# Optimization experiments

Measured on AMD Instinct MI355X. Metric: run time of the kernel, lower is better.

The kernel has to match this reference:

```python
import jax, jax.numpy as jnp
import numpy as np

N_HEAD = 16
EPS = 1e-5
ROPE_BASE = 10000.0


def setup_inputs() -> dict:
    key = jax.random.key(0)
    ks = jax.random.split(key, 6)
    B, T, C = 2, 2048, 1024
    s = 0.02  # typical GPT init scale
    return {
        "x": jax.random.normal(ks[0], (B, T, C), dtype=jnp.float32),
        "wq": jax.random.normal(ks[1], (C, C), dtype=jnp.float32) * s,
        "wk": jax.random.normal(ks[2], (C, C), dtype=jnp.float32) * s,
        "wv": jax.random.normal(ks[3], (C, C), dtype=jnp.float32) * s,
        "wproj": jax.random.normal(ks[4], (C, C), dtype=jnp.float32) * s,
        "g_rms": jnp.ones((C // N_HEAD,), dtype=jnp.float32),
    }


def reference(x, wq, wk, wv, wproj, g_rms):
    B, T, C = x.shape
    H = N_HEAD
    hd = C // H

    # QKV projections (torch Linear: y = x @ W.T), split into heads -> [B,T,H,hd]
    q = (x @ wq.T).reshape(B, T, H, hd)
    k = (x @ wk.T).reshape(B, T, H, hd)
    v = (x @ wv.T).reshape(B, T, H, hd)

    # RMSNorm over head_dim on q and k
    def rms(t):
        var = jnp.mean(t * t, axis=-1, keepdims=True) + EPS
        return g_rms * (t * jax.lax.rsqrt(var))

    q, k = rms(q), rms(k)

    # Rotary embeddings: cos/sin cached in bf16 in the original -> bf16 round-trip
    inv_freq = 1.0 / (ROPE_BASE ** (jnp.arange(0, hd, 2, dtype=jnp.float32) / hd))
    freqs = jnp.outer(jnp.arange(T, dtype=jnp.float32), inv_freq)  # [T, hd/2]
    cos = jnp.cos(freqs).astype(jnp.bfloat16).astype(jnp.float32)[None, :, None, :]
    sin = jnp.sin(freqs).astype(jnp.bfloat16).astype(jnp.float32)[None, :, None, :]

    def rope(u):
        d = hd // 2
        u1, u2 = u[..., :d], u[..., d:]
        return jnp.concatenate([u1 * cos + u2 * sin, -u1 * sin + u2 * cos], axis=-1)

    q, k = rope(q), rope(k)

    # Attention: float ones attn_mask => constant +1.0 bias (softmax-invariant);
    # NOT causal (is_causal defaults False); dropout_p = 0.
    qh = q.transpose(0, 2, 1, 3)  # [B,H,T,hd]
    kh = k.transpose(0, 2, 1, 3)
    vh = v.transpose(0, 2, 1, 3)
    scale = 1.0 / jnp.sqrt(jnp.float32(hd))
    scores = jnp.einsum('bhtd,bhsd->bhts', qh, kh) * scale + 1.0  # [B,H,T,T]
    attn = jax.nn.softmax(scores, axis=-1)
    y = jnp.einsum('bhts,bhsd->bhtd', attn, vh)

    y = y.transpose(0, 2, 1, 3).reshape(B, T, C)
    return y @ wproj.T
```

## Files before the change

### kernel.cpp

```cpp
#include <hip/hip_runtime.h>
#include <hip/hip_bf16.h>
#include <stdint.h>

typedef __attribute__((ext_vector_type(8))) short short8;
typedef __attribute__((ext_vector_type(4))) float f32x4;
typedef __attribute__((ext_vector_type(16))) float f32x16;
typedef __attribute__((ext_vector_type(4))) unsigned short ushort4v;
typedef __attribute__((ext_vector_type(4))) unsigned int uint4v;

#define TT 2048
#define HH 16
#define CCdim 1024
#define BT 4096
#define LOG2E 1.44269504088896f

__device__ inline unsigned short f2bf(float f) {
  unsigned u = __float_as_uint(f);
  u += 0x7FFF + ((u >> 16) & 1);
  return (unsigned short)(u >> 16);
}
__device__ inline float bf2f(unsigned short s) {
  return __uint_as_float(((unsigned)s) << 16);
}
__device__ inline unsigned pack2(float a, float b) {
  return (unsigned)f2bf(a) | ((unsigned)f2bf(b) << 16);
}
__device__ inline unsigned cvtpk(float lo, float hi) {
  unsigned r;
  asm("v_cvt_pk_bf16_f32 %0, %1, %2" : "=v"(r) : "v"(lo), "v"(hi));
  return r;
}
__device__ inline void plswap(unsigned &a, unsigned &b) {
  asm("v_permlane32_swap_b32 %0, %1" : "+v"(a), "+v"(b));
}

__device__ inline void gload16(const unsigned short* g, unsigned short* l) {
  __builtin_amdgcn_global_load_lds((const __attribute__((address_space(1))) void*)g,
                                   (__attribute__((address_space(3))) void*)l, 16, 0, 0);
}

#define VMB(N) do { asm volatile("s_waitcnt vmcnt(" #N ")" ::: "memory"); \
                    __builtin_amdgcn_s_barrier(); \
                    __builtin_amdgcn_sched_barrier(0); } while (0)

__global__ __launch_bounds__(256) void prep(const float* __restrict__ x, const float* __restrict__ wq,
                     const float* __restrict__ wk, const float* __restrict__ wv,
                     const float* __restrict__ wp, unsigned short* __restrict__ xb,
                     unsigned short* __restrict__ wqkv, unsigned short* __restrict__ wpb,
                     float2* __restrict__ tab) {
  long idx = ((long)blockIdx.x * 256 + threadIdx.x) * 4;
  const long NX = (long)BT * CCdim;
  const long NW = (long)CCdim * CCdim;
  auto cvt4 = [](const float* src, unsigned short* dst, long off) {
    float4 v = *(const float4*)(src + off);
    ushort4v o = { f2bf(v.x), f2bf(v.y), f2bf(v.z), f2bf(v.w) };
    *(ushort4v*)(dst + off) = o;
  };
  if (idx < NX) { cvt4(x, xb, idx); return; }
  idx -= NX;
  if (idx < NW) { cvt4(wq, wqkv, idx); return; }
  idx -= NW;
  if (idx < NW) { cvt4(wk, wqkv + NW, idx); return; }
  idx -= NW;
  if (idx < NW) { cvt4(wv, wqkv + 2 * NW, idx); return; }
  idx -= NW;
  if (idx < NW) { cvt4(wp, wpb, idx); return; }
  idx -= NW;
  if (idx < (long)TT * 32) {
#pragma unroll
    for (int j = 0; j < 4; ++j) {
      long e = idx + j;
      int t = (int)(e >> 5), i = (int)(e & 31);
      float invf = powf(10000.0f, -(float)i / 32.0f);
      float a = (float)t * invf;
      tab[e] = make_float2(bf2f(f2bf(cosf(a))), bf2f(f2bf(sinf(a))));
    }
  }
}

__global__ __launch_bounds__(256) void gemm_qkv(const unsigned short* __restrict__ A,
                                                const unsigned short* __restrict__ W,
                                                const float* __restrict__ g,
                                                const float2* __restrict__ tab,
                                                unsigned short* __restrict__ Qh,
                                                unsigned short* __restrict__ Kp,
                                                unsigned short* __restrict__ Vp) {
  __shared__ __align__(16) char smem[49152];
  unsigned short* const S0 = (unsigned short*)smem;
  unsigned short* const S1 = S0 + 8192;
  unsigned short* const S2 = S0 + 16384;
  typedef unsigned short (*Earr)[64][68];
  Earr E = (Earr)smem;
  const int K = 1024;
  const int tid = threadIdx.x;
  const int lane = tid & 63;
  const int wid = tid >> 6;
  const int wr = wid >> 1, wc = wid & 1;
  const int m0 = blockIdx.y * 128;
  const int n0 = blockIdx.x * 128;

  f32x4 acc[4][4] = {};

  const int srow0 = tid >> 2;
  const int cgrp = tid & 3;
  const int cd = (cgrp ^ ((srow0 >> 1) & 3)) * 8;
  const unsigned short* Arow0 = A + (long)(m0 + srow0) * K + cd;
  const unsigned short* Arow1 = A + (long)(m0 + srow0 + 64) * K + cd;
  const unsigned short* Wrow0 = W + (long)(n0 + srow0) * K + cd;
  const unsigned short* Wrow1 = W + (long)(n0 + srow0 + 64) * K + cd;

  auto stage = [&](unsigned short* Ab, int kt) {
    const int kof = kt * 32;
    gload16(Arow0 + kof, Ab + wid * 512);
    gload16(Arow1 + kof, Ab + 2048 + wid * 512);
    gload16(Wrow0 + kof, Ab + 4096 + wid * 512);
    gload16(Wrow1 + kof, Ab + 6144 + wid * 512);
  };
  auto compute = [&](const unsigned short* Ab) {
    const unsigned short* Wb = Ab + 4096;
    short8 af[4], bf[4];
#pragma unroll
    for (int mi = 0; mi < 4; ++mi) {
      int r = wr * 64 + mi * 16 + (lane & 15);
      af[mi] = *(const short8*)&Ab[r * 32 + (((lane >> 4) ^ ((r >> 1) & 3)) * 8)];
    }
#pragma unroll
    for (int nj = 0; nj < 4; ++nj) {
      int r = wc * 64 + nj * 16 + (lane & 15);
      bf[nj] = *(const short8*)&Wb[r * 32 + (((lane >> 4) ^ ((r >> 1) & 3)) * 8)];
    }
#pragma unroll
    for (int mi = 0; mi < 4; ++mi)
#pragma unroll
      for (int nj = 0; nj < 4; ++nj)
        acc[mi][nj] = __builtin_amdgcn_mfma_f32_16x16x32_bf16(af[mi], bf[nj], acc[mi][nj], 0, 0, 0);
  };

  stage(S0, 0);
  stage(S1, 1);
  for (int tb = 0; tb < 30; tb += 3) {
    VMB(4); stage(S2, tb + 2); compute(S0);
    VMB(4); stage(S0, tb + 3); compute(S1);
    VMB(4); stage(S1, tb + 4); compute(S2);
  }
  VMB(4); compute(S0);
  VMB(0); compute(S1);
  __syncthreads();

  const int type = blockIdx.x >> 3;
  const int c0 = n0 + wc * 64;
  const int b = m0 >> 11;
  const int t0w = (m0 & 2047) + wr * 64;
  const int bh = b * 16 + ((c0 >> 6) & 15);
  const int cl = lane & 15;
  const int hi4 = lane >> 4;

  if (type < 2) {
    float gv0 = g[cl], gv1 = g[cl + 16], gv2 = g[cl + 32], gv3 = g[cl + 48];
    const float qs = (type == 0) ? 0.125f * LOG2E : 1.0f;
#pragma unroll
    for (int mi = 0; mi < 4; ++mi)
#pragma unroll
      for (int j = 0; j < 4; ++j) {
        float x0 = acc[mi][0][j], x1 = acc[mi][1][j], x2 = acc[mi][2][j], x3 = acc[mi][3][j];
        float ss = x0 * x0 + x1 * x1 + x2 * x2 + x3 * x3;
        ss += __shfl_xor(ss, 1); ss += __shfl_xor(ss, 2);
        ss += __shfl_xor(ss, 4); ss += __shfl_xor(ss, 8);
        float ri = rsqrtf(ss * (1.0f / 64.0f) + 1e-5f);
        float xn0 = x0 * ri * gv0, xn1 = x1 * ri * gv1;
        float xn2 = x2 * ri * gv2, xn3 = x3 * ri * gv3;
        int t = t0w + mi * 16 + 4 * hi4 + j;
        float2 cs0 = tab[t * 32 + cl];
        float2 cs1 = tab[t * 32 + cl + 16];
        int lr = mi * 16 + 4 * hi4 + j;
        E[wid][lr][cl]      = f2bf((xn0 * cs0.x + xn2 * cs0.y) * qs);
        E[wid][lr][cl + 16] = f2bf((xn1 * cs1.x + xn3 * cs1.y) * qs);
        E[wid][lr][cl + 32] = f2bf((xn2 * cs0.x - xn0 * cs0.y) * qs);
        E[wid][lr][cl + 48] = f2bf((xn3 * cs1.x - xn1 * cs1.y) * qs);
      }
  } else {
#pragma unroll
    for (int mi = 0; mi < 4; ++mi)
#pragma unroll
      for (int j = 0; j < 4; ++j) {
        int lr = mi * 16 + 4 * hi4 + j;
        E[wid][lr][cl]      = f2bf(acc[mi][0][j]);
        E[wid][lr][cl + 16] = f2bf(acc[mi][1][j]);
        E[wid][lr][cl + 32] = f2bf(acc[mi][2][j]);
        E[wid][lr][cl + 48] = f2bf(acc[mi][3][j]);
      }
  }
  __syncthreads();

  if (type == 0) {
    for (int row = 0; row < 64; ++row) {
      int t = t0w + row;
      Qh[((long)bh * TT + t) * 64 + lane] = E[wid][row][lane];
    }
  } else if (type == 1) {
    for (int row = 0; row < 64; ++row) {
      int t = t0w + row;
      Kp[(((long)bh * 64 + (t >> 5)) * 4 + (lane >> 4)) * 512
         + ((t & 31) + 32 * ((lane >> 3) & 1)) * 8 + (lane & 7)] = E[wid][row][lane];
    }
  } else {
    unsigned short* base = Vp + ((long)bh * 64 + (t0w >> 5)) * 2048;
#pragma unroll
    for (int it = 0; it < 8; ++it) {
      int id = it * 64 + lane;
      int cc = it & 1, sd = (it >> 1) & 1, ttloc = (it >> 2) & 1;
      int d = sd * 32 + (lane & 31);
      int tl = ttloc * 32 + cc * 16 + (lane >> 5) * 8;
      short8 o;
#pragma unroll
      for (int jj = 0; jj < 8; ++jj) o[jj] = (short)E[wid][tl + jj][d];
      *(short8*)(base + (long)id * 8) = o;
    }
  }
}

__global__ __launch_bounds__(256) void gemm_bt(const unsigned short* __restrict__ A,
                                               const unsigned short* __restrict__ W,
                                               float* __restrict__ C, int ldc) {
  __shared__ __align__(16) unsigned short Sbuf[3][8192];
  unsigned short* const S0 = &Sbuf[0][0];
  unsigned short* const S1 = &Sbuf[1][0];
  unsigned short* const S2 = &Sbuf[2][0];
  const int K = 1024;
  const int tid = threadIdx.x;
  const int lane = tid & 63;
  const int wid = tid >> 6;
  const int wr = wid >> 1, wc = wid & 1;
  const int m0 = blockIdx.y * 128;
  const int n0 = blockIdx.x * 128;

  f32x4 acc[4][4] = {};

  const int srow0 = tid >> 2;
  const int cgrp = tid & 3;
  const int cd = (cgrp ^ ((srow0 >> 1) & 3)) * 8;
  const unsigned short* Arow0 = A + (long)(m0 + srow0) * K + cd;
  const unsigned short* Arow1 = A + (long)(m0 + srow0 + 64) * K + cd;
  const unsigned short* Wrow0 = W + (long)(n0 + srow0) * K + cd;
  const unsigned short* Wrow1 = W + (long)(n0 + srow0 + 64) * K + cd;

  auto stage = [&](unsigned short* Ab, int kt) {
    const int kof = kt * 32;
    gload16(Arow0 + kof, Ab + wid * 512);
    gload16(Arow1 + kof, Ab + 2048 + wid * 512);
    gload16(Wrow0 + kof, Ab + 4096 + wid * 512);
    gload16(Wrow1 + kof, Ab + 6144 + wid * 512);
  };
  auto compute = [&](const unsigned short* Ab) {
    const unsigned short* Wb = Ab + 4096;
    short8 af[4], bf[4];
#pragma unroll
    for (int mi = 0; mi < 4; ++mi) {
      int r = wr * 64 + mi * 16 + (lane & 15);
      af[mi] = *(const short8*)&Ab[r * 32 + (((lane >> 4) ^ ((r >> 1) & 3)) * 8)];
    }
#pragma unroll
    for (int nj = 0; nj < 4; ++nj) {
      int r = wc * 64 + nj * 16 + (lane & 15);
      bf[nj] = *(const short8*)&Wb[r * 32 + (((lane >> 4) ^ ((r >> 1) & 3)) * 8)];
    }
#pragma unroll
    for (int mi = 0; mi < 4; ++mi)
#pragma unroll
      for (int nj = 0; nj < 4; ++nj)
        acc[mi][nj] = __builtin_amdgcn_mfma_f32_16x16x32_bf16(af[mi], bf[nj], acc[mi][nj], 0, 0, 0);
  };

  stage(S0, 0);
  stage(S1, 1);
  for (int tb = 0; tb < 30; tb += 3) {
    VMB(4); stage(S2, tb + 2); compute(S0);
    VMB(4); stage(S0, tb + 3); compute(S1);
    VMB(4); stage(S1, tb + 4); compute(S2);
  }
  VMB(4); compute(S0);
  VMB(0); compute(S1);

#pragma unroll
  for (int mi = 0; mi < 4; ++mi)
#pragma unroll
    for (int nj = 0; nj < 4; ++nj)
#pragma unroll
      for (int j = 0; j < 4; ++j) {
        int rr = m0 + wr * 64 + mi * 16 + 4 * (lane >> 4) + j;
        int ncol = n0 + wc * 64 + nj * 16 + (lane & 15);
        C[(long)rr * ldc + ncol] = acc[mi][nj][j];
      }
}

__global__ __launch_bounds__(256, 3) void attn(const unsigned short* __restrict__ Qh,
                                               const unsigned short* __restrict__ Kp,
                                               const unsigned short* __restrict__ Vp,
                                               float* __restrict__ Opart,
                                               float* __restrict__ L) {
  const int lane = threadIdx.x & 63;
  const int wid = threadIdx.x >> 6;
  int bid = blockIdx.x;
  bid = (bid & 7) * 128 + (bid >> 3);
  const int w = bid * 4 + wid;
  const int qt = w & 63;
  const int half = (w >> 6) & 1;
  const int bh = w >> 7;
  const long bhT = (long)bh * TT;
  const int q0 = qt * 32;
  const int l31 = lane & 31;
  const int hk = (lane >> 5) * 8;

  short8 qf[4];
  {
    const unsigned short* qp = Qh + (bhT + q0 + l31) * 64 + hk;
#pragma unroll
    for (int c = 0; c < 4; ++c) qf[c] = *(const short8*)(qp + c * 16);
  }

  const unsigned short* kp = Kp + ((long)(bh * 64 + half * 32)) * 2048 + lane * 8;
  const unsigned short* vp = Vp + ((long)(bh * 64 + half * 32)) * 2048 + lane * 8;

  f32x16 oacc0 = {}, oacc1 = {};
  float ell = 0.f;

  short8 kA[4], vA0[2], vA1[2], kB[4], vB0[2], vB1[2];
#pragma unroll
  for (int c = 0; c < 4; ++c) kA[c] = *(const short8*)(kp + c * 512);
#pragma unroll
  for (int c = 0; c < 2; ++c) {
    vA0[c] = *(const short8*)(vp + c * 512);
    vA1[c] = *(const short8*)(vp + 1024 + c * 512);
  }

  auto body = [&](short8 (&kc)[4], short8 (&v0c)[2], short8 (&v1c)[2],
                  short8 (&knx)[4], short8 (&v0n)[2], short8 (&v1n)[2], int tn) {
    const unsigned short* kpn = kp + tn * 2048;
    const unsigned short* vpn = vp + tn * 2048;
#pragma unroll
    for (int c = 0; c < 4; ++c) knx[c] = *(const short8*)(kpn + c * 512);
#pragma unroll
    for (int c = 0; c < 2; ++c) {
      v0n[c] = *(const short8*)(vpn + c * 512);
      v1n[c] = *(const short8*)(vpn + 1024 + c * 512);
    }

    __builtin_amdgcn_s_setprio(1);
    f32x16 s = {};
#pragma unroll
    for (int c = 0; c < 4; ++c)
      s = __builtin_amdgcn_mfma_f32_32x32x16_bf16(kc[c], qf[c], s, 0, 0, 0);
    __builtin_amdgcn_s_setprio(0);

#pragma unroll
    for (int r = 0; r < 16; ++r) s[r] = __builtin_amdgcn_exp2f(s[r]);
    float t0 = s[0] + s[1], t1 = s[2] + s[3], t2s = s[4] + s[5], t3 = s[6] + s[7];
    float t4 = s[8] + s[9], t5 = s[10] + s[11], t6 = s[12] + s[13], t7 = s[14] + s[15];
    t0 += t1; t2s += t3; t4 += t5; t6 += t7;
    ell += (t0 + t2s) + (t4 + t6);

    unsigned a0 = cvtpk(s[0], s[1]),   a1 = cvtpk(s[2], s[3]);
    unsigned a2 = cvtpk(s[4], s[5]),   a3 = cvtpk(s[6], s[7]);
    unsigned a4 = cvtpk(s[8], s[9]),   a5 = cvtpk(s[10], s[11]);
    unsigned a6 = cvtpk(s[12], s[13]), a7 = cvtpk(s[14], s[15]);
    plswap(a0, a2); plswap(a1, a3); plswap(a4, a6); plswap(a5, a7);
    uint4v f0 = { a0, a1, a2, a3 };
    uint4v f1 = { a4, a5, a6, a7 };
    short8 pf0 = __builtin_bit_cast(short8, f0);
    short8 pf1 = __builtin_bit_cast(short8, f1);

    __builtin_amdgcn_s_setprio(1);
    oacc0 = __builtin_amdgcn_mfma_f32_32x32x16_bf16(v0c[0], pf0, oacc0, 0, 0, 0);
    oacc0 = __builtin_amdgcn_mfma_f32_32x32x16_bf16(v0c[1], pf1, oacc0, 0, 0, 0);
    oacc1 = __builtin_amdgcn_mfma_f32_32x32x16_bf16(v1c[0], pf0, oacc1, 0, 0, 0);
    oacc1 = __builtin_amdgcn_mfma_f32_32x32x16_bf16(v1c[1], pf1, oacc1, 0, 0, 0);
    __builtin_amdgcn_s_setprio(0);
  };

  for (int t = 0; t < 32; t += 2) {
    int t1 = t + 1;
    int t2 = (t < 30) ? (t + 2) : 31;
    body(kA, vA0, vA1, kB, vB0, vB1, t1);
    body(kB, vB0, vB1, kA, vA0, vA1, t2);
  }

  float ellf = ell + __shfl_xor(ell, 32);
  const long prow = (long)(half * 32 + bh) * TT + q0 + l31;
  float* orow = Opart + prow * 64;
  const int dhalf = 4 * (lane >> 5);
#pragma unroll
  for (int i = 0; i < 8; ++i) {
    int d = (2 * i & 3) + 8 * (i >> 1) + dhalf;
    *(float2*)&orow[d]      = make_float2(oacc0[2 * i], oacc0[2 * i + 1]);
    *(float2*)&orow[32 + d] = make_float2(oacc1[2 * i], oacc1[2 * i + 1]);
  }
  if (lane < 32) L[prow] = ellf;
}

__global__ __launch_bounds__(256) void combine(const float* __restrict__ Opart,
                                               const float* __restrict__ L,
                                               unsigned short* __restrict__ Y) {
  const long HALF = (long)32 * TT * 64;
  int idx = blockIdx.x * 256 + threadIdx.x;
  int row = idx >> 5;
  int d = (idx & 31) * 2;
  float2 o0 = *(const float2*)&Opart[(long)row * 64 + d];
  float2 o1 = *(const float2*)&Opart[HALF + (long)row * 64 + d];
  float rinv = 1.0f / (L[row] + L[65536 + row]);
  float ox = (o0.x + o1.x) * rinv;
  float oy = (o0.y + o1.y) * rinv;
  int bh = row >> 11, qrow = row & (TT - 1);
  int b = bh >> 4, h = bh & 15;
  *(unsigned*)&Y[((long)(b * TT + qrow)) * CCdim + h * 64 + d] = pack2(ox, oy);
}

extern "C" void kernel_launch(void* const* d_in, const int* in_sizes, int n_in,
                              void* d_out, int out_size, void* d_ws, size_t ws_size,
                              hipStream_t stream) {
  const float* x  = (const float*)d_in[0];
  const float* wq = (const float*)d_in[1];
  const float* wk = (const float*)d_in[2];
  const float* wv = (const float*)d_in[3];
  const float* wp = (const float*)d_in[4];
  const float* g  = (const float*)d_in[5];

  char* w = (char*)d_ws;
  unsigned short* xb   = (unsigned short*)w; w += (long)BT * CCdim * 2;
  unsigned short* wqkv = (unsigned short*)w; w += (long)3 * CCdim * CCdim * 2;
  unsigned short* wpb  = (unsigned short*)w; w += (long)CCdim * CCdim * 2;
  unsigned short* qh   = (unsigned short*)w; w += (long)BT * CCdim * 2;
  unsigned short* kp   = (unsigned short*)w; w += (long)BT * CCdim * 2;
  unsigned short* vp   = (unsigned short*)w; w += (long)BT * CCdim * 2;
  unsigned short* yb   = (unsigned short*)w; w += (long)BT * CCdim * 2;
  float2* tab          = (float2*)w;         w += (long)TT * 32 * 8;
  float* Opart         = (float*)w;          w += (long)64 * TT * 64 * 4;
  float* Lbuf          = (float*)w;          w += (long)64 * TT * 4;

  long total = ((long)BT * CCdim + 4L * CCdim * CCdim + (long)TT * 32) / 4;
  int pblocks = (int)((total + 255) / 256);
  prep<<<pblocks, 256, 0, stream>>>(x, wq, wk, wv, wp, xb, wqkv, wpb, tab);
  gemm_qkv<<<dim3(24, 32), 256, 0, stream>>>(xb, wqkv, g, tab, qh, kp, vp);
  attn<<<1024, 256, 0, stream>>>(qh, kp, vp, Opart, Lbuf);
  combine<<<8192, 256, 0, stream>>>(Opart, Lbuf, yb);
  gemm_bt<<<dim3(8, 32), 256, 0, stream>>>(yb, wpb, (float*)d_out, 1024);
}
```

Baseline: 134.2 us.

## Process two 32-row query tiles per wave in attention to reuse K/V loads

Each attention wave now handles 64 query rows instead of 32, holding two sets of Q fragments and four output accumulators, so every K/V fragment loaded from global memory feeds twice as many MFMAs. The grid is halved, the block remapping is adjusted, and launch bounds drop from 3 to 2 waves per SIMD to make room for the extra registers. This targets the global K/V load traffic per unit of compute, at the cost of lower occupancy and fewer blocks to hide latency.

```diff
diff --git a/kernel.cpp b/kernel.cpp
--- a/kernel.cpp
+++ b/kernel.cpp
@@ -293,7 +293,7 @@
       }
 }
 
-__global__ __launch_bounds__(256, 3) void attn(const unsigned short* __restrict__ Qh,
+__global__ __launch_bounds__(256, 2) void attn(const unsigned short* __restrict__ Qh,
                                                const unsigned short* __restrict__ Kp,
                                                const unsigned short* __restrict__ Vp,
                                                float* __restrict__ Opart,
@@ -301,28 +301,31 @@
   const int lane = threadIdx.x & 63;
   const int wid = threadIdx.x >> 6;
   int bid = blockIdx.x;
-  bid = (bid & 7) * 128 + (bid >> 3);
+  bid = (bid & 7) * 64 + (bid >> 3);
   const int w = bid * 4 + wid;
-  const int qt = w & 63;
-  const int half = (w >> 6) & 1;
-  const int bh = w >> 7;
+  const int qt = w & 31;
+  const int half = (w >> 5) & 1;
+  const int bh = w >> 6;
   const long bhT = (long)bh * TT;
-  const int q0 = qt * 32;
+  const int q0 = qt * 64;
   const int l31 = lane & 31;
   const int hk = (lane >> 5) * 8;
 
-  short8 qf[4];
+  short8 qf[4], qg[4];
   {
     const unsigned short* qp = Qh + (bhT + q0 + l31) * 64 + hk;
 #pragma unroll
-    for (int c = 0; c < 4; ++c) qf[c] = *(const short8*)(qp + c * 16);
+    for (int c = 0; c < 4; ++c) {
+      qf[c] = *(const short8*)(qp + c * 16);
+      qg[c] = *(const short8*)(qp + 2048 + c * 16);
+    }
   }
 
   const unsigned short* kp = Kp + ((long)(bh * 64 + half * 32)) * 2048 + lane * 8;
   const unsigned short* vp = Vp + ((long)(bh * 64 + half * 32)) * 2048 + lane * 8;
 
-  f32x16 oacc0 = {}, oacc1 = {};
-  float ell = 0.f;
+  f32x16 oacc0 = {}, oacc1 = {}, oacc2 = {}, oacc3 = {};
+  float ell = 0.f, ell2 = 0.f;
 
   short8 kA[4], vA0[2], vA1[2], kB[4], vB0[2], vB1[2];
 #pragma unroll
@@ -346,18 +349,30 @@
     }
 
     __builtin_amdgcn_s_setprio(1);
-    f32x16 s = {};
-#pragma unroll
-    for (int c = 0; c < 4; ++c)
-      s = __builtin_amdgcn_mfma_f32_32x32x16_bf16(kc[c], qf[c], s, 0, 0, 0);
+    f32x16 s = {}, s2 = {};
+#pragma unroll
+    for (int c = 0; c < 4; ++c) {
+      s  = __builtin_amdgcn_mfma_f32_32x32x16_bf16(kc[c], qf[c], s, 0, 0, 0);
+      s2 = __builtin_amdgcn_mfma_f32_32x32x16_bf16(kc[c], qg[c], s2, 0, 0, 0);
+    }
     __builtin_amdgcn_s_setprio(0);
 
 #pragma unroll
     for (int r = 0; r < 16; ++r) s[r] = __builtin_amdgcn_exp2f(s[r]);
-    float t0 = s[0] + s[1], t1 = s[2] + s[3], t2s = s[4] + s[5], t3 = s[6] + s[7];
-    float t4 = s[8] + s[9], t5 = s[10] + s[11], t6 = s[12] + s[13], t7 = s[14] + s[15];
-    t0 += t1; t2s += t3; t4 += t5; t6 += t7;
-    ell += (t0 + t2s) + (t4 + t6);
+#pragma unroll
+    for (int r = 0; r < 16; ++r) s2[r] = __builtin_amdgcn_exp2f(s2[r]);
+    {
+      float t0 = s[0] + s[1], t1 = s[2] + s[3], t2s = s[4] + s[5], t3 = s[6] + s[7];
+      float t4 = s[8] + s[9], t5 = s[10] + s[11], t6 = s[12] + s[13], t7 = s[14] + s[15];
+      t0 += t1; t2s += t3; t4 += t5; t6 += t7;
+      ell += (t0 + t2s) + (t4 + t6);
+    }
+    {
+      float t0 = s2[0] + s2[1], t1 = s2[2] + s2[3], t2s = s2[4] + s2[5], t3 = s2[6] + s2[7];
+      float t4 = s2[8] + s2[9], t5 = s2[10] + s2[11], t6 = s2[12] + s2[13], t7 = s2[14] + s2[15];
+      t0 += t1; t2s += t3; t4 += t5; t6 += t7;
+      ell2 += (t0 + t2s) + (t4 + t6);
+    }
 
     unsigned a0 = cvtpk(s[0], s[1]),   a1 = cvtpk(s[2], s[3]);
     unsigned a2 = cvtpk(s[4], s[5]),   a3 = cvtpk(s[6], s[7]);
@@ -369,11 +384,25 @@
     short8 pf0 = __builtin_bit_cast(short8, f0);
     short8 pf1 = __builtin_bit_cast(short8, f1);
 
+    unsigned b0 = cvtpk(s2[0], s2[1]),   b1 = cvtpk(s2[2], s2[3]);
+    unsigned b2 = cvtpk(s2[4], s2[5]),   b3 = cvtpk(s2[6], s2[7]);
+    unsigned b4 = cvtpk(s2[8], s2[9]),   b5 = cvtpk(s2[10], s2[11]);
+    unsigned b6 = cvtpk(s2[12], s2[13]), b7 = cvtpk(s2[14], s2[15]);
+    plswap(b0, b2); plswap(b1, b3); plswap(b4, b6); plswap(b5, b7);
+    uint4v g0 = { b0, b1, b2, b3 };
+    uint4v g1 = { b4, b5, b6, b7 };
+    short8 pg0 = __builtin_bit_cast(short8, g0);
+    short8 pg1 = __builtin_bit_cast(short8, g1);
+
     __builtin_amdgcn_s_setprio(1);
     oacc0 = __builtin_amdgcn_mfma_f32_32x32x16_bf16(v0c[0], pf0, oacc0, 0, 0, 0);
     oacc0 = __builtin_amdgcn_mfma_f32_32x32x16_bf16(v0c[1], pf1, oacc0, 0, 0, 0);
     oacc1 = __builtin_amdgcn_mfma_f32_32x32x16_bf16(v1c[0], pf0, oacc1, 0, 0, 0);
     oacc1 = __builtin_amdgcn_mfma_f32_32x32x16_bf16(v1c[1], pf1, oacc1, 0, 0, 0);
+    oacc2 = __builtin_amdgcn_mfma_f32_32x32x16_bf16(v0c[0], pg0, oacc2, 0, 0, 0);
+    oacc2 = __builtin_amdgcn_mfma_f32_32x32x16_bf16(v0c[1], pg1, oacc2, 0, 0, 0);
+    oacc3 = __builtin_amdgcn_mfma_f32_32x32x16_bf16(v1c[0], pg0, oacc3, 0, 0, 0);
+    oacc3 = __builtin_amdgcn_mfma_f32_32x32x16_bf16(v1c[1], pg1, oacc3, 0, 0, 0);
     __builtin_amdgcn_s_setprio(0);
   };
 
@@ -384,17 +413,21 @@
     body(kB, vB0, vB1, kA, vA0, vA1, t2);
   }
 
-  float ellf = ell + __shfl_xor(ell, 32);
+  float ellf  = ell + __shfl_xor(ell, 32);
+  float ellf2 = ell2 + __shfl_xor(ell2, 32);
   const long prow = (long)(half * 32 + bh) * TT + q0 + l31;
-  float* orow = Opart + prow * 64;
+  float* orow  = Opart + prow * 64;
+  float* orow2 = orow + 32 * 64;
   const int dhalf = 4 * (lane >> 5);
 #pragma unroll
   for (int i = 0; i < 8; ++i) {
     int d = (2 * i & 3) + 8 * (i >> 1) + dhalf;
-    *(float2*)&orow[d]      = make_float2(oacc0[2 * i], oacc0[2 * i + 1]);
-    *(float2*)&orow[32 + d] = make_float2(oacc1[2 * i], oacc1[2 * i + 1]);
-  }
-  if (lane < 32) L[prow] = ellf;
+    *(float2*)&orow[d]       = make_float2(oacc0[2 * i], oacc0[2 * i + 1]);
+    *(float2*)&orow[32 + d]  = make_float2(oacc1[2 * i], oacc1[2 * i + 1]);
+    *(float2*)&orow2[d]      = make_float2(oacc2[2 * i], oacc2[2 * i + 1]);
+    *(float2*)&orow2[32 + d] = make_float2(oacc3[2 * i], oacc3[2 * i + 1]);
+  }
+  if (lane < 32) { L[prow] = ellf; L[prow + 32] = ellf2; }
 }
 
 __global__ __launch_bounds__(256) void combine(const float* __restrict__ Opart,
@@ -440,7 +473,7 @@
   int pblocks = (int)((total + 255) / 256);
   prep<<<pblocks, 256, 0, stream>>>(x, wq, wk, wv, wp, xb, wqkv, wpb, tab);
   gemm_qkv<<<dim3(24, 32), 256, 0, stream>>>(xb, wqkv, g, tab, qh, kp, vp);
-  attn<<<1024, 256, 0, stream>>>(qh, kp, vp, Opart, Lbuf);
+  attn<<<512, 256, 0, stream>>>(qh, kp, vp, Opart, Lbuf);
   combine<<<8192, 256, 0, stream>>>(Opart, Lbuf, yb);
   gemm_bt<<<dim3(8, 32), 256, 0, stream>>>(yb, wpb, (float*)d_out, 1024);
 }
```

After: 127.4 us. -5.1%, faster.
